# Optimization experiments

Hardware: AMD Instinct MI355X
Metric: run time of the kernel (lower is better)

## Reference

```python
import jax, jax.numpy as jnp
import numpy as np

CHANNELS = 1024
N_HEADS = 16
N_EMBD = 512
H_DIM = CHANNELS // N_HEADS


def setup_inputs() -> dict:
    key = jax.random.key(0)
    ks = jax.random.split(key, 10)
    b, hw = 16, 4096
    s = 0.02
    return {
        "x": jax.random.normal(ks[0], (b, hw, CHANNELS), dtype=jnp.float32),
        "p": jax.random.normal(ks[1], (b, 77, N_EMBD), dtype=jnp.float32),
        "Wq": jax.random.normal(ks[2], (CHANNELS, CHANNELS), dtype=jnp.float32) * s,
        "bq": jnp.zeros((CHANNELS,), dtype=jnp.float32),
        "Wk": jax.random.normal(ks[3], (N_EMBD, CHANNELS), dtype=jnp.float32) * s,
        "bk": jnp.zeros((CHANNELS,), dtype=jnp.float32),
        "Wv": jax.random.normal(ks[4], (N_EMBD, CHANNELS), dtype=jnp.float32) * s,
        "bv": jnp.zeros((CHANNELS,), dtype=jnp.float32),
        "Ww": jax.random.normal(ks[5], (CHANNELS, CHANNELS), dtype=jnp.float32) * s,
        "bw": jnp.zeros((CHANNELS,), dtype=jnp.float32),
    }


def reference(x, p, Wq, bq, Wk, bk, Wv, bv, Ww, bw):
    b, hw, c = x.shape
    # Linear projections (torch Linear: y = x @ W^T + b; here weights stored as (in, out))
    q = x @ Wq + bq                      # (b, hw, c)
    k = p @ Wk + bk                      # (b, 77, c)
    v = p @ Wv + bv                      # (b, 77, c)
    q = q.reshape(b, hw, N_HEADS, H_DIM)
    k = k.reshape(b, 77, N_HEADS, H_DIM)
    v = v.reshape(b, 77, N_HEADS, H_DIM)
    scale = 1.0 / jnp.sqrt(jnp.asarray(H_DIM, dtype=x.dtype))
    # scores: (b, heads, hw, 77)
    scores = jnp.einsum("bqhd,bkhd->bhqk", q, k) * scale
    attn = jax.nn.softmax(scores, axis=-1)
    out = jnp.einsum("bhqk,bkhd->bqhd", attn, v).reshape(b, hw, c)
    return out @ Ww + bw
```

## Files before the change

kernel.cpp:

```cpp
#include <hip/hip_runtime.h>
#include <cstdint>
#include <type_traits>

typedef uint16_t u16;
typedef uint32_t u32;
typedef __attribute__((ext_vector_type(4))) float f32x4;
typedef __attribute__((ext_vector_type(8))) __bf16 vbf8;
typedef __attribute__((ext_vector_type(8))) short vs8;

template <typename T, typename = void>
struct CanMfma : std::false_type {};
template <typename T>
struct CanMfma<T, std::void_t<decltype(__builtin_amdgcn_mfma_f32_16x16x32_bf16(
    std::declval<T>(), std::declval<T>(), std::declval<f32x4>(), 0, 0, 0))>>
    : std::true_type {};
typedef std::conditional_t<CanMfma<vbf8>::value, vbf8, vs8> frag_t;

__device__ __forceinline__ f32x4 mfma_bf16(frag_t a, frag_t b, f32x4 c) {
  return __builtin_amdgcn_mfma_f32_16x16x32_bf16(a, b, c, 0, 0, 0);
}

__device__ __forceinline__ u16 f2bf(float f) {
  u32 u = __builtin_bit_cast(u32, f);
  u32 r = (u + 0x7FFFu + ((u >> 16) & 1u)) >> 16;
  return (u16)r;
}

__device__ __forceinline__ void gload_lds16(const void* g, void* l) {
  __builtin_amdgcn_global_load_lds(
      (const __attribute__((address_space(1))) void*)g,
      (__attribute__((address_space(3))) void*)l, 16, 0, 0);
}

#define SB0() __builtin_amdgcn_sched_barrier(0)

__device__ __forceinline__ void transpose_body(
    const float* __restrict__ in, u16* __restrict__ out, int K, int N,
    int k0, int n0, float (*tile)[33]) {
  const int tr = threadIdx.x >> 5, tc = threadIdx.x & 31;
#pragma unroll
  for (int i = 0; i < 4; ++i)
    tile[tr + i * 8][tc] = in[(size_t)(k0 + tr + i * 8) * N + (n0 + tc)];
  __syncthreads();
#pragma unroll
  for (int i = 0; i < 4; ++i)
    out[(size_t)(n0 + tr + i * 8) * K + (k0 + tc)] = f2bf(tile[tc][tr + i * 8]);
}

__global__ __launch_bounds__(256) void prep_kernel(
    const float* __restrict__ x, const float* __restrict__ p,
    const float* __restrict__ Wq, const float* __restrict__ Ww,
    const float* __restrict__ Wk, const float* __restrict__ Wv,
    u16* __restrict__ x_bf, u16* __restrict__ p_bf,
    u16* __restrict__ wq_t, u16* __restrict__ ww_t, u16* __restrict__ wkv_t) {
  __shared__ float tile[32][33];
  const int bid = blockIdx.x;
  if (bid < 32768) {
    const size_t i = (size_t)bid * 256 + threadIdx.x;
    const float4 a  = ((const float4*)x)[i * 2];
    const float4 b2 = ((const float4*)x)[i * 2 + 1];
    uint4 o;
    o.x = (u32)f2bf(a.x)  | ((u32)f2bf(a.y)  << 16);
    o.y = (u32)f2bf(a.z)  | ((u32)f2bf(a.w)  << 16);
    o.z = (u32)f2bf(b2.x) | ((u32)f2bf(b2.y) << 16);
    o.w = (u32)f2bf(b2.z) | ((u32)f2bf(b2.w) << 16);
    ((uint4*)x_bf)[i] = o;
  } else if (bid < 33076) {
    const int i = (bid - 32768) * 256 + threadIdx.x;
    if (i < 78848) {
      const float4 a  = ((const float4*)p)[(size_t)i * 2];
      const float4 b2 = ((const float4*)p)[(size_t)i * 2 + 1];
      uint4 o;
      o.x = (u32)f2bf(a.x)  | ((u32)f2bf(a.y)  << 16);
      o.y = (u32)f2bf(a.z)  | ((u32)f2bf(a.w)  << 16);
      o.z = (u32)f2bf(b2.x) | ((u32)f2bf(b2.y) << 16);
      o.w = (u32)f2bf(b2.z) | ((u32)f2bf(b2.w) << 16);
      ((uint4*)p_bf)[(size_t)i] = o;
    }
  } else if (bid < 35124) {
    const bool isQ = bid < 34100;
    const int r = (bid - (isQ ? 33076 : 34100));
    transpose_body(isQ ? Wq : Ww, isQ ? wq_t : ww_t, 1024, 1024,
                   (r & 31) * 32, (r >> 5) * 32, tile);
  } else {
    const bool isK = bid < 35636;
    const int r = (bid - (isK ? 35124 : 35636));
    transpose_body(isK ? Wk : Wv, isK ? wkv_t : (wkv_t + 1024 * 512), 512, 1024,
                   (r & 15) * 32, (r >> 4) * 32, tile);
  }
}

template <bool OUT_BF16>
__global__ __launch_bounds__(256) void gemm_bt(
    const u16* __restrict__ A, const u16* __restrict__ Bt,
    const float* __restrict__ biasA, const float* __restrict__ biasB,
    void* __restrict__ Cout,
    int M, int N, int K, int Mtiles, int Ntiles) {
  __shared__ char Al[2][128 * 32 * 2];
  __shared__ char Bl[2][128 * 32 * 2];

  const int nwg = Mtiles * Ntiles;
  int bid = (int)blockIdx.x;
  bid = (bid & 7) * (nwg >> 3) + (bid >> 3);
  const int mt = bid / Ntiles, nt = bid % Ntiles;
  const int m0 = mt * 128, n0 = nt * 128;

  const int tid = (int)threadIdx.x;
  const int lane = tid & 63;
  const int wv = tid >> 6;
  const int wm = wv & 1, wn = wv >> 1;
  const int lr = lane & 15, lg = lane >> 4;
  const int rsub = lane >> 2;
  const int slot = lane & 3;
  const int rb0 = n0 + rsub;

  auto stage = [&](int buf, int t) {
    const int k0 = t << 5;
#pragma unroll
    for (int c = 0; c < 2; ++c) {
      const int ci = c * 4 + wv;
      int rra = m0 + ci * 16 + rsub;
      if (rra >= M) rra = M - 1;
      gload_lds16(A + (size_t)rra * K + k0 + slot * 8, Al[buf] + ci * 1024);
      const int rrb = rb0 + ci * 16;
      gload_lds16(Bt + (size_t)rrb * K + k0 + slot * 8, Bl[buf] + ci * 1024);
    }
  };

  f32x4 zero4 = {0.f, 0.f, 0.f, 0.f};
  f32x4 acc[4][4];
#pragma unroll
  for (int i = 0; i < 4; ++i)
#pragma unroll
    for (int j = 0; j < 4; ++j) acc[i][j] = zero4;

  const int nk = K >> 5;
  int cur = 0;
  stage(0, 0);
  __syncthreads();

  for (int t = 0; t < nk; ++t) {
    if (t + 1 < nk) stage(cur ^ 1, t + 1);
    frag_t af[4], bf[4];
#pragma unroll
    for (int i = 0; i < 4; ++i) {
      af[i] = *(const frag_t*)(Al[cur] + (wm * 64 + i * 16 + lr) * 64 + lg * 16);
      bf[i] = *(const frag_t*)(Bl[cur] + (wn * 64 + i * 16 + lr) * 64 + lg * 16);
    }
#pragma unroll
    for (int i = 0; i < 4; ++i)
#pragma unroll
      for (int j = 0; j < 4; ++j)
        acc[i][j] = mfma_bf16(af[i], bf[j], acc[i][j]);
    __syncthreads();
    cur ^= 1;
  }

#pragma unroll
  for (int j = 0; j < 4; ++j) {
    const int col = n0 + wn * 64 + j * 16 + lr;
    const float bv = (col < 1024) ? biasA[col] : biasB[col - 1024];
#pragma unroll
    for (int i = 0; i < 4; ++i) {
      const int rbase = m0 + wm * 64 + i * 16 + lg * 4;
#pragma unroll
      for (int r = 0; r < 4; ++r) {
        const int row = rbase + r;
        const float val = acc[i][j][r] + bv;
        if constexpr (OUT_BF16) {
          u32 me = f2bf(val);
          u32 other = __shfl_xor(me, 1);
          if ((lane & 1) == 0 && row < M) {
            *(u32*)((u16*)Cout + (size_t)row * N + col) = me | (other << 16);
          }
        } else {
          if (row < M) ((float*)Cout)[(size_t)row * N + col] = val;
        }
      }
    }
  }
}

template <bool OUT_BF16>
__global__ __launch_bounds__(512, 1) void gemm8p(
    const u16* __restrict__ A, const u16* __restrict__ Bt,
    const float* __restrict__ bias, void* __restrict__ Cout,
    int M, int N, int K) {
  __shared__ u16 Al[2][256 * 64];
  __shared__ u16 Bl[2][256 * 64];

  const int Ntiles = N >> 8;
  const int nwg = (M >> 8) * Ntiles;
  int bid = (int)blockIdx.x;
  bid = (bid & 7) * (nwg >> 3) + (bid >> 3);
  const int mt = bid / Ntiles, ntl = bid % Ntiles;
  const int m0 = mt << 8, n0 = ntl << 8;

  const int tid = (int)threadIdx.x;
  const int lane = tid & 63;
  const int wid = tid >> 6;
  const int wm = wid >> 2, wn = wid & 3;
  const int lr = lane & 15, lg = lane >> 4;
  const int sslot = (lane & 7) ^ (lane >> 3);
  const int lrow = lane >> 3;

  auto stageA = [&](u16* dst, int half, int t) {
#pragma unroll
    for (int sub = 0; sub < 2; ++sub) {
      const int s = half + sub * 2;
      const u16* g = A + (size_t)(m0 + s * 64 + wid * 8 + lrow) * K + t * 64 + sslot * 8;
      u16* l = dst + (s & 1) * 8192 + (s >> 1) * 4096 + wid * 512;
      gload_lds16(g, l);
    }
  };
  auto stageB = [&](u16* dst, int half, int t) {
#pragma unroll
    for (int sub = 0; sub < 2; ++sub) {
      const int ub = wid * 16 + sub * 8;
      const int r = n0 + (ub >> 5) * 64 + half * 32 + (ub & 31) + lrow;
      const u16* g = Bt + (size_t)r * K + t * 64 + sslot * 8;
      u16* l = dst + half * 8192 + ub * 64;
      gload_lds16(g, l);
    }
  };

  auto ldsA = [&](const u16* base, int r, int ks) -> frag_t {
    const int off = ((r >> 6) & 1) * 8192 + (r >> 7) * 4096 + (r & 63) * 64 +
                    ((((ks) << 2) + lg) ^ (r & 7)) * 8;
    return *(const frag_t*)(base + off);
  };
  auto ldsB = [&](const u16* base, int r, int ks) -> frag_t {
    const int off = ((r >> 5) & 1) * 8192 + (r >> 6) * 2048 + (r & 31) * 64 +
                    ((((ks) << 2) + lg) ^ (r & 7)) * 8;
    return *(const frag_t*)(base + off);
  };

  f32x4 acc[8][4];
#pragma unroll
  for (int i = 0; i < 8; ++i)
#pragma unroll
    for (int j = 0; j < 4; ++j)
#pragma unroll
      for (int r = 0; r < 4; ++r) acc[i][j][r] = 0.f;

  frag_t aR[4][2], b0R[2][2], b1R[2][2];
  auto mmq = [&](frag_t (&bb)[2][2], int mo, int no) {
    __builtin_amdgcn_s_setprio(1);
#pragma unroll
    for (int i = 0; i < 4; ++i)
#pragma unroll
      for (int j = 0; j < 2; ++j) {
        acc[mo + i][no + j] = mfma_bf16(aR[i][0], bb[j][0], acc[mo + i][no + j]);
        acc[mo + i][no + j] = mfma_bf16(aR[i][1], bb[j][1], acc[mo + i][no + j]);
      }
    __builtin_amdgcn_s_setprio(0);
  };

  const int nt = K >> 6;
  const int arow = wm * 128 + lr;
  const int brow = wn * 64 + lr;

  stageA(&Al[0][0], 0, 0); stageA(&Al[0][0], 1, 0);
  stageB(&Bl[0][0], 0, 0); stageB(&Bl[0][0], 1, 0);
  stageA(&Al[1][0], 0, 1);
  stageB(&Bl[1][0], 0, 1); stageB(&Bl[1][0], 1, 1);
  asm volatile("s_waitcnt vmcnt(6)" ::: "memory");
  __builtin_amdgcn_s_barrier();

  for (int t = 0; t < nt; ++t) {
    const int cur = t & 1;
    const u16* bA = &Al[cur][0];
    const u16* bB = &Bl[cur][0];
#pragma unroll
    for (int i = 0; i < 4; ++i) {
      aR[i][0] = ldsA(bA, arow + i * 16, 0);
      aR[i][1] = ldsA(bA, arow + i * 16, 1);
    }
#pragma unroll
    for (int j = 0; j < 2; ++j) {
      b0R[j][0] = ldsB(bB, brow + j * 16, 0);
      b0R[j][1] = ldsB(bB, brow + j * 16, 1);
    }
    if (t + 1 < nt) stageA(&Al[cur ^ 1][0], 1, t + 1);
    asm volatile("s_waitcnt lgkmcnt(8)" ::: "memory");
    SB0();
    __builtin_amdgcn_s_barrier();
    asm volatile("s_waitcnt lgkmcnt(0)" ::: "memory");
    SB0();
    mmq(b0R, 0, 0);
    __builtin_amdgcn_s_barrier();
#pragma unroll
    for (int j = 0; j < 2; ++j) {
      b1R[j][0] = ldsB(bB, brow + 32 + j * 16, 0);
      b1R[j][1] = ldsB(bB, brow + 32 + j * 16, 1);
    }
    if (t + 2 < nt) stageA(&Al[cur][0], 0, t + 2);
    SB0();
    __builtin_amdgcn_s_barrier();
    asm volatile("s_waitcnt lgkmcnt(0)" ::: "memory");
    SB0();
    mmq(b1R, 0, 2);
    __builtin_amdgcn_s_barrier();
#pragma unroll
    for (int i = 0; i < 4; ++i) {
      aR[i][0] = ldsA(bA, arow + 64 + i * 16, 0);
      aR[i][1] = ldsA(bA, arow + 64 + i * 16, 1);
    }
    if (t + 2 < nt) stageB(&Bl[cur][0], 0, t + 2);
    SB0();
    __builtin_amdgcn_s_barrier();
    asm volatile("s_waitcnt lgkmcnt(0)" ::: "memory");
    SB0();
    mmq(b1R, 4, 2);
    __builtin_amdgcn_s_barrier();
    if (t + 2 < nt) stageB(&Bl[cur][0], 1, t + 2);
    mmq(b0R, 4, 0);
    if (t + 2 < nt)
      asm volatile("s_waitcnt vmcnt(6)" ::: "memory");
    else if (t + 1 < nt)
      asm volatile("s_waitcnt vmcnt(0)" ::: "memory");
    if (t + 1 < nt) __builtin_amdgcn_s_barrier();
  }

  float bvv[4];
#pragma unroll
  for (int nf = 0; nf < 4; ++nf) bvv[nf] = bias[n0 + wn * 64 + nf * 16 + lr];
#pragma unroll
  for (int mf = 0; mf < 8; ++mf) {
    const int rbase = m0 + wm * 128 + mf * 16 + lg * 4;
#pragma unroll
    for (int rr = 0; rr < 4; ++rr) {
      const int row = rbase + rr;
#pragma unroll
      for (int nf = 0; nf < 4; ++nf) {
        const int cb = n0 + wn * 64 + nf * 16;
        const float val = acc[mf][nf][rr] + bvv[nf];
        if constexpr (OUT_BF16) {
          u32 me = f2bf(val);
          u32 d0 = me | (__shfl_xor(me, 1) << 16);
          u32 d1 = __shfl_xor(d0, 2);
          if ((lane & 3) == 0) {
            uint2 o; o.x = d0; o.y = d1;
            *(uint2*)((u16*)Cout + (size_t)row * N + cb + (lr & 12)) = o;
          }
        } else {
          float v0 = val;
          float v1 = __shfl_xor(v0, 1);
          float v2 = __shfl_xor(v0, 2);
          float v3 = __shfl_xor(v1, 2);
          if ((lane & 3) == 0) {
            float4 o; o.x = v0; o.y = v1; o.z = v2; o.w = v3;
            *(float4*)((float*)Cout + (size_t)row * N + cb + (lr & 12)) = o;
          }
        }
      }
    }
  }
}

__global__ __launch_bounds__(256) void attn_kernel(
    const u16* __restrict__ Q, const u16* __restrict__ KV,
    u16* __restrict__ O) {
  __shared__ u16 Kl[96][72];
  __shared__ u16 Vt[64][104];

  const int bid = blockIdx.x;
  const int qt0 = bid & 15;
  const int h = (bid >> 4) & 15;
  const int b = bid >> 8;
  const int tid = threadIdx.x;

#pragma unroll
  for (int it = 0; it < 3; ++it) {
    const int idx = tid + it * 256;
    const int key = idx >> 3, s = idx & 7;
    uint4 val{0u, 0u, 0u, 0u};
    if (key < 77)
      val = *(const uint4*)(KV + ((size_t)(b * 77 + key)) * 2048 + h * 64 + s * 8);
    *(uint4*)(&Kl[key][s * 8]) = val;
  }
#pragma unroll
  for (int it = 0; it < 3; ++it) {
    const int idx = tid + it * 256;
    if (idx < 616) {
      const int key = idx >> 3, s = idx & 7;
      const uint4 v4 = *(const uint4*)(KV + ((size_t)(b * 77 + key)) * 2048 +
                                       1024 + h * 64 + s * 8);
      const u16* e = (const u16*)&v4;
#pragma unroll
      for (int j = 0; j < 8; ++j) Vt[s * 8 + j][key] = e[j];
    }
  }
#pragma unroll
  for (int it = 0; it < 5; ++it) {
    const int idx = tid + it * 256;
    if (idx < 1216) {
      const int d = idx / 19, kk = 77 + idx % 19;
      Vt[d][kk] = 0;
    }
  }
  __syncthreads();

  const int lane = tid & 63;
  const int wv = tid >> 6;
  const int lr = lane & 15;
  const int lg = lane >> 4;
  f32x4 zero4 = {0.f, 0.f, 0.f, 0.f};

  for (int q4 = 0; q4 < 4; ++q4) {
    const int qt = qt0 * 4 + q4;

    const size_t qrow = (size_t)(b * 4096 + qt * 64 + wv * 16 + lr) * 1024 + h * 64;
    frag_t qf[2];
#pragma unroll
    for (int ks = 0; ks < 2; ++ks)
      qf[ks] = *(const frag_t*)(Q + qrow + ks * 32 + lg * 8);

    f32x4 sa[5] = {zero4, zero4, zero4, zero4, zero4};
#pragma unroll
    for (int ks = 0; ks < 2; ++ks) {
#pragma unroll
      for (int kt = 0; kt < 5; ++kt) {
        frag_t kf = *(const frag_t*)(&Kl[kt * 16 + lr][ks * 32 + lg * 8]);
        sa[kt] = mfma_bf16(kf, qf[ks], sa[kt]);
      }
    }

    float p[5][4];
    float mx = -3.0e38f;
#pragma unroll
    for (int kt = 0; kt < 5; ++kt)
#pragma unroll
      for (int r = 0; r < 4; ++r) {
        const int key = kt * 16 + lg * 4 + r;
        float s = sa[kt][r] * 0.125f;
        if (key >= 77) s = -3.0e38f;
        p[kt][r] = s;
        mx = fmaxf(mx, s);
      }
    mx = fmaxf(mx, __shfl_xor(mx, 16));
    mx = fmaxf(mx, __shfl_xor(mx, 32));
    float sum = 0.f;
#pragma unroll
    for (int kt = 0; kt < 5; ++kt)
#pragma unroll
      for (int r = 0; r < 4; ++r) {
        const float e = __expf(p[kt][r] - mx);
        p[kt][r] = e;
        sum += e;
      }
    sum += __shfl_xor(sum, 16);
    sum += __shfl_xor(sum, 32);
    const float rden = 1.0f / sum;
#pragma unroll
    for (int kt = 0; kt < 5; ++kt)
#pragma unroll
      for (int r = 0; r < 4; ++r) p[kt][r] *= rden;

    union FP { frag_t v; u16 e[8]; };
    frag_t pa[3];
#pragma unroll
    for (int kb = 0; kb < 3; ++kb) {
      FP f;
#pragma unroll
      for (int j = 0; j < 8; ++j) {
        const int kt = 2 * kb + (j >> 2);
        f.e[j] = (kt < 5) ? f2bf(p[kt][j & 3]) : (u16)0;
      }
      pa[kb] = f.v;
    }

    f32x4 oa[4] = {zero4, zero4, zero4, zero4};
#pragma unroll
    for (int nt = 0; nt < 4; ++nt) {
      const int d = nt * 16 + lr;
#pragma unroll
      for (int kb = 0; kb < 3; ++kb) {
        const int key0 = kb * 32 + lg * 4;
        FP vb;
        *(uint2*)(&vb.e[0]) = *(const uint2*)(&Vt[d][key0]);
        *(uint2*)(&vb.e[4]) = *(const uint2*)(&Vt[d][key0 + 16]);
        oa[nt] = mfma_bf16(pa[kb], vb.v, oa[nt]);
      }
    }

#pragma unroll
    for (int nt = 0; nt < 4; ++nt)
#pragma unroll
      for (int r = 0; r < 4; ++r) {
        const int qr = wv * 16 + lg * 4 + r;
        u32 me = f2bf(oa[nt][r]);
        u32 other = __shfl_xor(me, 1);
        if ((lane & 1) == 0) {
          *(u32*)(O + ((size_t)(b * 4096 + qt * 64 + qr)) * 1024 + h * 64 +
                  nt * 16 + lr) = me | (other << 16);
        }
      }
  }
}

extern "C" void kernel_launch(void* const* d_in, const int* in_sizes, int n_in,
                              void* d_out, int out_size, void* d_ws, size_t ws_size,
                              hipStream_t stream) {
  const float* x  = (const float*)d_in[0];
  const float* p  = (const float*)d_in[1];
  const float* Wq = (const float*)d_in[2];
  const float* bq = (const float*)d_in[3];
  const float* Wk = (const float*)d_in[4];
  const float* bk = (const float*)d_in[5];
  const float* Wv = (const float*)d_in[6];
  const float* bv = (const float*)d_in[7];
  const float* Ww = (const float*)d_in[8];
  const float* bw = (const float*)d_in[9];

  char* ws = (char*)d_ws;
  if (ws_size < 281034752ULL) return;

  u16* x_bf  = (u16*)(ws + 0);
  u16* q_bf  = (u16*)(ws + 134217728);
  u16* wq_t  = (u16*)(ws + 268435456);
  u16* ww_t  = (u16*)(ws + 270532608);
  u16* wkv_t = (u16*)(ws + 272629760);
  u16* p_bf  = (u16*)(ws + 274726912);
  u16* kv_bf = (u16*)(ws + 275988480);

  prep_kernel<<<36148, 256, 0, stream>>>(x, p, Wq, Ww, Wk, Wv,
                                         x_bf, p_bf, wq_t, ww_t, wkv_t);
  gemm_bt<true><<<160, 256, 0, stream>>>(p_bf, wkv_t, bk, bv, kv_bf,
                                         1232, 2048, 512, 10, 16);
  gemm8p<true><<<1024, 512, 0, stream>>>(x_bf, wq_t, bq, q_bf, 65536, 1024, 1024);
  attn_kernel<<<4096, 256, 0, stream>>>(q_bf, kv_bf, x_bf);
  gemm8p<false><<<1024, 512, 0, stream>>>(x_bf, ww_t, bw, d_out, 65536, 1024, 1024);
}
```

Before: 514.5 us.

## Fuse Q projection GEMM with cross-attention in one kernel epilogue

Replaces the separate Q-projection GEMM and attention kernel with one kernel. Each 256x256 output tile of the Q GEMM (4 heads) is turned to bf16 in LDS and immediately run through attention against K/V staged in shared memory. This removes writing and re-reading the 128MB Q intermediate and one launch, at the cost of a longer, more LDS-hungry epilogue (about 138KB of shared memory at one block per CU) that serialises attention after the GEMM main loop.

```diff
diff --git a/kernel.cpp b/kernel.cpp
--- a/kernel.cpp
+++ b/kernel.cpp
@@ -358,144 +358,324 @@
   }
 }
 
-__global__ __launch_bounds__(256) void attn_kernel(
-    const u16* __restrict__ Q, const u16* __restrict__ KV,
-    u16* __restrict__ O) {
-  __shared__ u16 Kl[96][72];
-  __shared__ u16 Vt[64][104];
-
-  const int bid = blockIdx.x;
-  const int qt0 = bid & 15;
-  const int h = (bid >> 4) & 15;
-  const int b = bid >> 8;
-  const int tid = threadIdx.x;
-
-#pragma unroll
-  for (int it = 0; it < 3; ++it) {
-    const int idx = tid + it * 256;
-    const int key = idx >> 3, s = idx & 7;
-    uint4 val{0u, 0u, 0u, 0u};
-    if (key < 77)
-      val = *(const uint4*)(KV + ((size_t)(b * 77 + key)) * 2048 + h * 64 + s * 8);
-    *(uint4*)(&Kl[key][s * 8]) = val;
+__global__ __launch_bounds__(512, 1) void gemm8p_fa(
+    const u16* __restrict__ A, const u16* __restrict__ Bt,
+    const float* __restrict__ bias, const u16* __restrict__ KV,
+    u16* __restrict__ Oout, int M, int N, int K) {
+  __shared__ u16 smem[70656];
+  u16* Al0 = smem;
+  u16* Bl0 = smem + 32768;
+
+  const int Ntiles = N >> 8;
+  const int nwg = (M >> 8) * Ntiles;
+  int bid = (int)blockIdx.x;
+  bid = (bid & 7) * (nwg >> 3) + (bid >> 3);
+  const int mt = bid / Ntiles, ntl = bid % Ntiles;
+  const int m0 = mt << 8, n0 = ntl << 8;
+
+  const int tid = (int)threadIdx.x;
+  const int lane = tid & 63;
+  const int wid = tid >> 6;
+  const int wm = wid >> 2, wn = wid & 3;
+  const int lr = lane & 15, lg = lane >> 4;
+  const int sslot = (lane & 7) ^ (lane >> 3);
+  const int lrow = lane >> 3;
+
+  auto stageA = [&](u16* dst, int half, int t) {
+#pragma unroll
+    for (int sub = 0; sub < 2; ++sub) {
+      const int s = half + sub * 2;
+      const u16* g = A + (size_t)(m0 + s * 64 + wid * 8 + lrow) * K + t * 64 + sslot * 8;
+      u16* l = dst + (s & 1) * 8192 + (s >> 1) * 4096 + wid * 512;
+      gload_lds16(g, l);
+    }
+  };
+  auto stageB = [&](u16* dst, int half, int t) {
+#pragma unroll
+    for (int sub = 0; sub < 2; ++sub) {
+      const int ub = wid * 16 + sub * 8;
+      const int r = n0 + (ub >> 5) * 64 + half * 32 + (ub & 31) + lrow;
+      const u16* g = Bt + (size_t)r * K + t * 64 + sslot * 8;
+      u16* l = dst + half * 8192 + ub * 64;
+      gload_lds16(g, l);
+    }
+  };
+  auto ldsA = [&](const u16* base, int r, int ks) -> frag_t {
+    const int off = ((r >> 6) & 1) * 8192 + (r >> 7) * 4096 + (r & 63) * 64 +
+                    ((((ks) << 2) + lg) ^ (r & 7)) * 8;
+    return *(const frag_t*)(base + off);
+  };
+  auto ldsB = [&](const u16* base, int r, int ks) -> frag_t {
+    const int off = ((r >> 5) & 1) * 8192 + (r >> 6) * 2048 + (r & 31) * 64 +
+                    ((((ks) << 2) + lg) ^ (r & 7)) * 8;
+    return *(const frag_t*)(base + off);
+  };
+
+  f32x4 acc[8][4];
+#pragma unroll
+  for (int i = 0; i < 8; ++i)
+#pragma unroll
+    for (int j = 0; j < 4; ++j)
+#pragma unroll
+      for (int r = 0; r < 4; ++r) acc[i][j][r] = 0.f;
+
+  frag_t aR[4][2], b0R[2][2], b1R[2][2];
+  auto mmq = [&](frag_t (&bb)[2][2], int mo, int no) {
+    __builtin_amdgcn_s_setprio(1);
+#pragma unroll
+    for (int i = 0; i < 4; ++i)
+#pragma unroll
+      for (int j = 0; j < 2; ++j) {
+        acc[mo + i][no + j] = mfma_bf16(aR[i][0], bb[j][0], acc[mo + i][no + j]);
+        acc[mo + i][no + j] = mfma_bf16(aR[i][1], bb[j][1], acc[mo + i][no + j]);
+      }
+    __builtin_amdgcn_s_setprio(0);
+  };
+
+  const int nt = K >> 6;
+  const int arow = wm * 128 + lr;
+  const int brow = wn * 64 + lr;
+
+  stageA(Al0, 0, 0); stageA(Al0, 1, 0);
+  stageB(Bl0, 0, 0); stageB(Bl0, 1, 0);
+  stageA(Al0 + 16384, 0, 1);
+  stageB(Bl0 + 16384, 0, 1); stageB(Bl0 + 16384, 1, 1);
+  asm volatile("s_waitcnt vmcnt(6)" ::: "memory");
+  __builtin_amdgcn_s_barrier();
+
+  for (int t = 0; t < nt; ++t) {
+    const int cur = t & 1;
+    const u16* bA = Al0 + cur * 16384;
+    const u16* bB = Bl0 + cur * 16384;
+#pragma unroll
+    for (int i = 0; i < 4; ++i) {
+      aR[i][0] = ldsA(bA, arow + i * 16, 0);
+      aR[i][1] = ldsA(bA, arow + i * 16, 1);
+    }
+#pragma unroll
+    for (int j = 0; j < 2; ++j) {
+      b0R[j][0] = ldsB(bB, brow + j * 16, 0);
+      b0R[j][1] = ldsB(bB, brow + j * 16, 1);
+    }
+    if (t + 1 < nt) stageA(Al0 + (cur ^ 1) * 16384, 1, t + 1);
+    asm volatile("s_waitcnt lgkmcnt(8)" ::: "memory");
+    SB0();
+    __builtin_amdgcn_s_barrier();
+    asm volatile("s_waitcnt lgkmcnt(0)" ::: "memory");
+    SB0();
+    mmq(b0R, 0, 0);
+    __builtin_amdgcn_s_barrier();
+#pragma unroll
+    for (int j = 0; j < 2; ++j) {
+      b1R[j][0] = ldsB(bB, brow + 32 + j * 16, 0);
+      b1R[j][1] = ldsB(bB, brow + 32 + j * 16, 1);
+    }
+    if (t + 2 < nt) stageA(Al0 + cur * 16384, 0, t + 2);
+    SB0();
+    __builtin_amdgcn_s_barrier();
+    asm volatile("s_waitcnt lgkmcnt(0)" ::: "memory");
+    SB0();
+    mmq(b1R, 0, 2);
+    __builtin_amdgcn_s_barrier();
+#pragma unroll
+    for (int i = 0; i < 4; ++i) {
+      aR[i][0] = ldsA(bA, arow + 64 + i * 16, 0);
+      aR[i][1] = ldsA(bA, arow + 64 + i * 16, 1);
+    }
+    if (t + 2 < nt) stageB(Bl0 + cur * 16384, 0, t + 2);
+    SB0();
+    __builtin_amdgcn_s_barrier();
+    asm volatile("s_waitcnt lgkmcnt(0)" ::: "memory");
+    SB0();
+    mmq(b1R, 4, 2);
+    __builtin_amdgcn_s_barrier();
+    if (t + 2 < nt) stageB(Bl0 + cur * 16384, 1, t + 2);
+    mmq(b0R, 4, 0);
+    if (t + 2 < nt)
+      asm volatile("s_waitcnt vmcnt(6)" ::: "memory");
+    else if (t + 1 < nt)
+      asm volatile("s_waitcnt vmcnt(0)" ::: "memory");
+    if (t + 1 < nt) __builtin_amdgcn_s_barrier();
   }
-#pragma unroll
-  for (int it = 0; it < 3; ++it) {
-    const int idx = tid + it * 256;
-    if (idx < 616) {
-      const int key = idx >> 3, s = idx & 7;
-      const uint4 v4 = *(const uint4*)(KV + ((size_t)(b * 77 + key)) * 2048 +
-                                       1024 + h * 64 + s * 8);
-      const u16* e = (const u16*)&v4;
-#pragma unroll
-      for (int j = 0; j < 8; ++j) Vt[s * 8 + j][key] = e[j];
-    }
-  }
-#pragma unroll
-  for (int it = 0; it < 5; ++it) {
-    const int idx = tid + it * 256;
-    if (idx < 1216) {
-      const int d = idx / 19, kk = 77 + idx % 19;
-      Vt[d][kk] = 0;
+
+  __syncthreads();
+
+  u16* Kl4 = smem;
+  u16* Vt4 = smem + 27648;
+  u16* Qw  = smem + 27648 + 26624;
+
+  const int b = m0 >> 12;
+  const int hbase = n0 >> 6;
+  {
+    const int sq = tid >> 8;
+    const int t2 = tid & 255;
+#pragma unroll
+    for (int hh = 0; hh < 2; ++hh) {
+      const int hl = sq * 2 + hh;
+      const int hg = hbase + hl;
+      u16* KlH = Kl4 + hl * 6912;
+      u16* VtH = Vt4 + hl * 6656;
+#pragma unroll
+      for (int it = 0; it < 3; ++it) {
+        const int idx = t2 + it * 256;
+        const int key = idx >> 3, s = idx & 7;
+        uint4 val{0u, 0u, 0u, 0u};
+        if (key < 77)
+          val = *(const uint4*)(KV + ((size_t)(b * 77 + key)) * 2048 + hg * 64 + s * 8);
+        *(uint4*)(KlH + key * 72 + s * 8) = val;
+      }
+#pragma unroll
+      for (int it = 0; it < 3; ++it) {
+        const int idx = t2 + it * 256;
+        if (idx < 616) {
+          const int key = idx >> 3, s = idx & 7;
+          const uint4 v4 = *(const uint4*)(KV + ((size_t)(b * 77 + key)) * 2048 +
+                                           1024 + hg * 64 + s * 8);
+          const u16* e = (const u16*)&v4;
+#pragma unroll
+          for (int j = 0; j < 8; ++j) VtH[(s * 8 + j) * 104 + key] = e[j];
+        }
+      }
+#pragma unroll
+      for (int it = 0; it < 5; ++it) {
+        const int idx = t2 + it * 256;
+        if (idx < 1216) {
+          const int d = idx / 19, kk = 77 + idx % 19;
+          VtH[d * 104 + kk] = 0;
+        }
+      }
     }
   }
   __syncthreads();
 
-  const int lane = tid & 63;
-  const int wv = tid >> 6;
-  const int lr = lane & 15;
-  const int lg = lane >> 4;
+  const u16* KlH = Kl4 + wn * 6912;
+  const u16* VtH = Vt4 + wn * 6656;
+  u16* QwW = Qw + wid * 2048;
+  const int qbase = (m0 & 4095) + wm * 128;
+  const int hg = hbase + wn;
+  float bvv[4];
+#pragma unroll
+  for (int nf = 0; nf < 4; ++nf) bvv[nf] = bias[hg * 64 + nf * 16 + lr];
   f32x4 zero4 = {0.f, 0.f, 0.f, 0.f};
 
-  for (int q4 = 0; q4 < 4; ++q4) {
-    const int qt = qt0 * 4 + q4;
-
-    const size_t qrow = (size_t)(b * 4096 + qt * 64 + wv * 16 + lr) * 1024 + h * 64;
-    frag_t qf[2];
-#pragma unroll
-    for (int ks = 0; ks < 2; ++ks)
-      qf[ks] = *(const frag_t*)(Q + qrow + ks * 32 + lg * 8);
-
-    f32x4 sa[5] = {zero4, zero4, zero4, zero4, zero4};
-#pragma unroll
-    for (int ks = 0; ks < 2; ++ks) {
-#pragma unroll
-      for (int kt = 0; kt < 5; ++kt) {
-        frag_t kf = *(const frag_t*)(&Kl[kt * 16 + lr][ks * 32 + lg * 8]);
-        sa[kt] = mfma_bf16(kf, qf[ks], sa[kt]);
-      }
-    }
-
-    float p[5][4];
-    float mx = -3.0e38f;
-#pragma unroll
-    for (int kt = 0; kt < 5; ++kt)
-#pragma unroll
-      for (int r = 0; r < 4; ++r) {
-        const int key = kt * 16 + lg * 4 + r;
-        float s = sa[kt][r] * 0.125f;
-        if (key >= 77) s = -3.0e38f;
-        p[kt][r] = s;
-        mx = fmaxf(mx, s);
-      }
-    mx = fmaxf(mx, __shfl_xor(mx, 16));
-    mx = fmaxf(mx, __shfl_xor(mx, 32));
-    float sum = 0.f;
-#pragma unroll
-    for (int kt = 0; kt < 5; ++kt)
-#pragma unroll
-      for (int r = 0; r < 4; ++r) {
-        const float e = __expf(p[kt][r] - mx);
-        p[kt][r] = e;
-        sum += e;
-      }
-    sum += __shfl_xor(sum, 16);
-    sum += __shfl_xor(sum, 32);
-    const float rden = 1.0f / sum;
-#pragma unroll
-    for (int kt = 0; kt < 5; ++kt)
-#pragma unroll
-      for (int r = 0; r < 4; ++r) p[kt][r] *= rden;
-
-    union FP { frag_t v; u16 e[8]; };
-    frag_t pa[3];
-#pragma unroll
-    for (int kb = 0; kb < 3; ++kb) {
-      FP f;
-#pragma unroll
-      for (int j = 0; j < 8; ++j) {
-        const int kt = 2 * kb + (j >> 2);
-        f.e[j] = (kt < 5) ? f2bf(p[kt][j & 3]) : (u16)0;
-      }
-      pa[kb] = f.v;
-    }
-
-    f32x4 oa[4] = {zero4, zero4, zero4, zero4};
-#pragma unroll
-    for (int nt = 0; nt < 4; ++nt) {
-      const int d = nt * 16 + lr;
+#pragma unroll
+  for (int sub = 0; sub < 4; ++sub) {
+#pragma unroll
+    for (int mm = 0; mm < 2; ++mm) {
+      const int mf = sub * 2 + mm;
+#pragma unroll
+      for (int rr = 0; rr < 4; ++rr) {
+        const int r2 = mm * 16 + lg * 4 + rr;
+#pragma unroll
+        for (int nf = 0; nf < 4; ++nf) {
+          const float val = acc[mf][nf][rr] + bvv[nf];
+          u32 me = f2bf(val);
+          u32 d0 = me | (__shfl_xor(me, 1) << 16);
+          u32 d1 = __shfl_xor(d0, 2);
+          u32 d2 = __shfl_xor(d0, 4);
+          u32 d3 = __shfl_xor(d1, 4);
+          if ((lane & 7) == 0) {
+            const int s3 = nf * 2 + (lr >> 3);
+            uint4 o; o.x = d0; o.y = d1; o.z = d2; o.w = d3;
+            *(uint4*)(QwW + r2 * 64 + ((s3 ^ (r2 & 7)) * 8)) = o;
+          }
+        }
+      }
+    }
+    asm volatile("s_waitcnt lgkmcnt(0)" ::: "memory");
+    SB0();
+
+#pragma unroll
+    for (int g = 0; g < 2; ++g) {
+      const int r2q = g * 16 + lr;
+      frag_t qf[2];
+#pragma unroll
+      for (int ks = 0; ks < 2; ++ks)
+        qf[ks] = *(const frag_t*)(QwW + r2q * 64 + (((ks * 4 + lg) ^ (r2q & 7)) * 8));
+
+      f32x4 sa[5] = {zero4, zero4, zero4, zero4, zero4};
+#pragma unroll
+      for (int ks = 0; ks < 2; ++ks) {
+#pragma unroll
+        for (int kt = 0; kt < 5; ++kt) {
+          frag_t kf = *(const frag_t*)(KlH + (kt * 16 + lr) * 72 + ks * 32 + lg * 8);
+          sa[kt] = mfma_bf16(kf, qf[ks], sa[kt]);
+        }
+      }
+
+      float p[5][4];
+      float mx = -3.0e38f;
+#pragma unroll
+      for (int kt = 0; kt < 5; ++kt)
+#pragma unroll
+        for (int r = 0; r < 4; ++r) {
+          const int key = kt * 16 + lg * 4 + r;
+          float s = sa[kt][r] * 0.125f;
+          if (key >= 77) s = -3.0e38f;
+          p[kt][r] = s;
+          mx = fmaxf(mx, s);
+        }
+      mx = fmaxf(mx, __shfl_xor(mx, 16));
+      mx = fmaxf(mx, __shfl_xor(mx, 32));
+      float sum = 0.f;
+#pragma unroll
+      for (int kt = 0; kt < 5; ++kt)
+#pragma unroll
+        for (int r = 0; r < 4; ++r) {
+          const float e = __expf(p[kt][r] - mx);
+          p[kt][r] = e;
+          sum += e;
+        }
+      sum += __shfl_xor(sum, 16);
+      sum += __shfl_xor(sum, 32);
+      const float rden = 1.0f / sum;
+#pragma unroll
+      for (int kt = 0; kt < 5; ++kt)
+#pragma unroll
+        for (int r = 0; r < 4; ++r) p[kt][r] *= rden;
+
+      union FP { frag_t v; u16 e[8]; };
+      frag_t pa[3];
 #pragma unroll
       for (int kb = 0; kb < 3; ++kb) {
-        const int key0 = kb * 32 + lg * 4;
-        FP vb;
-        *(uint2*)(&vb.e[0]) = *(const uint2*)(&Vt[d][key0]);
-        *(uint2*)(&vb.e[4]) = *(const uint2*)(&Vt[d][key0 + 16]);
-        oa[nt] = mfma_bf16(pa[kb], vb.v, oa[nt]);
-      }
-    }
-
-#pragma unroll
-    for (int nt = 0; nt < 4; ++nt)
-#pragma unroll
-      for (int r = 0; r < 4; ++r) {
-        const int qr = wv * 16 + lg * 4 + r;
-        u32 me = f2bf(oa[nt][r]);
-        u32 other = __shfl_xor(me, 1);
-        if ((lane & 1) == 0) {
-          *(u32*)(O + ((size_t)(b * 4096 + qt * 64 + qr)) * 1024 + h * 64 +
-                  nt * 16 + lr) = me | (other << 16);
-        }
-      }
+        FP f;
+#pragma unroll
+        for (int j = 0; j < 8; ++j) {
+          const int kt = 2 * kb + (j >> 2);
+          f.e[j] = (kt < 5) ? f2bf(p[kt][j & 3]) : (u16)0;
+        }
+        pa[kb] = f.v;
+      }
+
+      f32x4 oa[4] = {zero4, zero4, zero4, zero4};
+#pragma unroll
+      for (int ot = 0; ot < 4; ++ot) {
+        const int d = ot * 16 + lr;
+#pragma unroll
+        for (int kb = 0; kb < 3; ++kb) {
+          const int key0 = kb * 32 + lg * 4;
+          FP vb;
+          *(uint2*)(&vb.e[0]) = *(const uint2*)(VtH + d * 104 + key0);
+          *(uint2*)(&vb.e[4]) = *(const uint2*)(VtH + d * 104 + key0 + 16);
+          oa[ot] = mfma_bf16(pa[kb], vb.v, oa[ot]);
+        }
+      }
+
+#pragma unroll
+      for (int ot = 0; ot < 4; ++ot)
+#pragma unroll
+        for (int r = 0; r < 4; ++r) {
+          const int qr = qbase + sub * 32 + g * 16 + lg * 4 + r;
+          u32 me = f2bf(oa[ot][r]);
+          u32 other = __shfl_xor(me, 1);
+          if ((lane & 1) == 0) {
+            *(u32*)(Oout + ((size_t)(b * 4096 + qr)) * 1024 + hg * 64 +
+                    ot * 16 + lr) = me | (other << 16);
+          }
+        }
+    }
+    asm volatile("s_waitcnt lgkmcnt(0)" ::: "memory");
+    SB0();
   }
 }
 
@@ -517,7 +697,7 @@
   if (ws_size < 281034752ULL) return;
 
   u16* x_bf  = (u16*)(ws + 0);
-  u16* q_bf  = (u16*)(ws + 134217728);
+  u16* ao_bf = (u16*)(ws + 134217728);
   u16* wq_t  = (u16*)(ws + 268435456);
   u16* ww_t  = (u16*)(ws + 270532608);
   u16* wkv_t = (u16*)(ws + 272629760);
@@ -528,7 +708,7 @@
                                          x_bf, p_bf, wq_t, ww_t, wkv_t);
   gemm_bt<true><<<160, 256, 0, stream>>>(p_bf, wkv_t, bk, bv, kv_bf,
                                          1232, 2048, 512, 10, 16);
-  gemm8p<true><<<1024, 512, 0, stream>>>(x_bf, wq_t, bq, q_bf, 65536, 1024, 1024);
-  attn_kernel<<<4096, 256, 0, stream>>>(q_bf, kv_bf, x_bf);
-  gemm8p<false><<<1024, 512, 0, stream>>>(x_bf, ww_t, bw, d_out, 65536, 1024, 1024);
-}
+  gemm8p_fa<<<1024, 512, 0, stream>>>(x_bf, wq_t, bq, kv_bf, ao_bf,
+                                      65536, 1024, 1024);
+  gemm8p<false><<<1024, 512, 0, stream>>>(ao_bf, ww_t, bw, d_out, 65536, 1024, 1024);
+}
```

Measured after the change: 571.2 us. 11.0% more time.
